# Kernel optimization log

Measured on AMD Instinct MI355X. Metric: run time of the kernel, lower is better.

## Reference

```python
import jax, jax.numpy as jnp
import numpy as np

NEG = -1.0e9  # matches the -1000000000.0 masking constant in the torch source


def setup_inputs() -> dict:
    key = jax.random.key(0)
    k1, k2, k3, k4 = jax.random.split(key, 4)
    B, N, M, D = 32, 2048, 512, 128
    sequence1 = jax.random.normal(k1, (B, N, D), dtype=jnp.float32)
    sequence2 = jax.random.normal(k2, (B, M, D), dtype=jnp.float32)
    sequence1_mask = jax.random.randint(k3, (B, N), 0, 2, dtype=jnp.int32)
    sequence2_mask = jax.random.randint(k4, (B, M), 0, 2, dtype=jnp.int32)
    return {
        "sequence1": sequence1,
        "sequence2": sequence2,
        "sequence1_mask": sequence1_mask,
        "sequence2_mask": sequence2_mask,
    }


def reference(sequence1, sequence2, sequence1_mask, sequence2_mask):
    # sequence1: [B, n, d] (context), sequence2: [B, m, d] (question)
    dt = sequence1.dtype
    m1 = sequence1_mask.astype(dt)  # [B, n]
    m2 = sequence2_mask.astype(dt)  # [B, m]

    # DotProduct similarity over the (virtually) tiled tensors -> [B, n, m].
    # Fused: no [B,n,m,d] intermediates.
    S = jnp.einsum('bnd,bmd->bnm', sequence1, sequence2)

    # masked softmax over sequence2 positions (context-to-question attention)
    a2 = jax.nn.softmax(S + (1.0 - m2)[:, None, :] * NEG, axis=-1)  # [B, n, m]
    seq1_seq2_attention = jnp.einsum('bnm,bmd->bnd', a2, sequence2)

    # one-shot question-to-context attention: masked max over m, softmax over n
    s1 = jnp.max(S * m2[:, None, :] + (1.0 - m2)[:, None, :] * NEG, axis=-1)  # [B, n]
    a1 = jax.nn.softmax(s1 + (1.0 - m1) * NEG, axis=-1)  # [B, n]
    seq2_seq1_attention = jnp.einsum('bn,bnd->bd', a1, sequence1)  # [B, d]

    return (seq1_seq2_attention, a2, seq2_seq1_attention, a1)
```

## Files before the change

kernel.cpp:

```cpp
#include <hip/hip_runtime.h>
#include <stdint.h>

#define NEGC (-1.0e9f)

typedef __attribute__((ext_vector_type(8))) short bf16x8;
typedef __attribute__((ext_vector_type(4))) float f32x4;

__device__ __align__(16) unsigned short g_S2H[32u * 512u * 128u];
__device__ __align__(16) unsigned short g_S2L[32u * 512u * 128u];
__device__ __align__(16) unsigned short g_VF[32u * 128u * 512u];
__device__ float g_a1log[32 * 2048];

__device__ __forceinline__ unsigned short f2bf(float f) {
    union { float f; unsigned int u; } v; v.f = f;
    unsigned int r = v.u + 0x7fffu + ((v.u >> 16) & 1u);
    return (unsigned short)(r >> 16);
}
__device__ __forceinline__ float bf2f(unsigned short h) {
    union { float f; unsigned int u; } v; v.u = ((unsigned int)h) << 16;
    return v.f;
}

__device__ __forceinline__ void gl_lds16(const void* g, void* l) {
    __builtin_amdgcn_global_load_lds(
        (const __attribute__((address_space(1))) unsigned int*)g,
        (__attribute__((address_space(3))) unsigned int*)l, 16, 0, 0);
}

__global__ __launch_bounds__(256) void k_prep(const float* __restrict__ seq2) {
    __shared__ unsigned short Lh[32 * 136];
    const int b = blockIdx.x >> 4, c = blockIdx.x & 15, t = threadIdx.x;
    const int m0 = c * 32;

    const float4* src = (const float4*)(seq2 + (size_t)(b * 512 + m0) * 128);
    ushort4* dh = (ushort4*)(g_S2H + (size_t)(b * 512 + m0) * 128);
    ushort4* dl = (ushort4*)(g_S2L + (size_t)(b * 512 + m0) * 128);
#pragma unroll
    for (int p = 0; p < 4; ++p) {
        int idx = p * 256 + t;
        int row = idx >> 5, c4 = idx & 31;
        float4 v = src[idx];
        float vs[4] = {v.x, v.y, v.z, v.w};
        unsigned short hh[4], ll[4];
#pragma unroll
        for (int i = 0; i < 4; ++i) { hh[i] = f2bf(vs[i]); ll[i] = f2bf(vs[i] - bf2f(hh[i])); }
        ushort4 uh{hh[0], hh[1], hh[2], hh[3]};
        ushort4 ul{ll[0], ll[1], ll[2], ll[3]};
        dh[idx] = uh;
        dl[idx] = ul;
#pragma unroll
        for (int i = 0; i < 4; ++i) Lh[row * 136 + c4 * 4 + i] = hh[i];
    }
    __syncthreads();

    {
        const int l = t & 63, q = (t >> 4) & 3, fr = t & 15;
        const int ms = m0 >> 5;
#pragma unroll
        for (int pass = 0; pass < 2; ++pass) {
            int id = pass * 4 + (t >> 6);
            int wcd = id >> 2, cc = id & 3;
            int d = wcd * 64 + cc * 16 + fr;
            unsigned short pk[8];
#pragma unroll
            for (int j = 0; j < 8; ++j) pk[j] = Lh[(q * 8 + j) * 136 + d];
            size_t chunk = (size_t)b * 65536 + (size_t)wcd * 32768
                         + (size_t)ms * 2048 + cc * 512 + l * 8;
            *(bf16x8*)(g_VF + chunk) = *(bf16x8*)pk;
        }
    }
}

#define LDS_TOTAL 32768

__global__ __launch_bounds__(256, 4) void bidir_main(
    const float* __restrict__ seq1,
    const int* __restrict__ m1, const int* __restrict__ m2,
    float* __restrict__ out0, float* __restrict__ a2out,
    float* __restrict__ out2)
{
    __shared__ __align__(16) char smem[LDS_TOTAL];

    const int t = threadIdx.x, lane = t & 63, w = t >> 6;
    const int wr = w >> 1, wc = w & 1, q = lane >> 4, fr = lane & 15;
    const int orig = blockIdx.x;
    const int swzb = (orig & 7) * 256 + (orig >> 3);
    const int b = swzb >> 6, n0 = (swzb & 63) << 5;

    float* REDm = (float*)(smem);
    float* REDs = (float*)(smem + 256);

    if (orig == 0) {
#pragma unroll
        for (int i = 0; i < 16; ++i) out2[i * 256 + t] = 0.f;
    }

    auto stageK = [&](int buf, int kt) {
        const unsigned short* sb = (w < 2) ? g_S2H : g_S2L;
        const int h = w & 1;
        const char* srcb = (const char*)(sb + (size_t)(b * 512 + h * 256 + kt * 16) * 128);
        char* dstb = smem + buf * 16384 + (w >> 1) * 8192 + h * 4096;
#pragma unroll
        for (int i = 0; i < 4; ++i) {
            int r = i * 4 + q;
            int so = r * 256 + ((fr * 16) ^ ((r & 7) << 4));
            gl_lds16(srcb + so, dstb + i * 1024);
        }
    };

    stageK(0, 0);

    bf16x8 ah[4], al[4];
    {
        const float* qp = seq1 + (size_t)(b * 2048 + n0 + wr * 16 + fr) * 128;
#pragma unroll
        for (int ks = 0; ks < 4; ++ks) {
            float4 v0 = *(const float4*)(qp + ks * 32 + q * 8);
            float4 v1 = *(const float4*)(qp + ks * 32 + q * 8 + 4);
            float vs[8] = {v0.x, v0.y, v0.z, v0.w, v1.x, v1.y, v1.z, v1.w};
            unsigned short hh[8], ll[8];
#pragma unroll
            for (int j = 0; j < 8; ++j) { hh[j] = f2bf(vs[j]); ll[j] = f2bf(vs[j] - bf2f(hh[j])); }
            ah[ks] = *(bf16x8*)hh;
            al[ks] = *(bf16x8*)ll;
        }
    }

    f32x4 acc[8][2];
#pragma unroll
    for (int i = 0; i < 8; ++i) {
        acc[i][0] = (f32x4){0.f, 0.f, 0.f, 0.f};
        acc[i][1] = (f32x4){0.f, 0.f, 0.f, 0.f};
    }

    __syncthreads();

#pragma unroll
    for (int kt = 0; kt < 16; ++kt) {
        if (kt < 15) stageK((kt + 1) & 1, kt + 1);
        {
            const char* KH = smem + (kt & 1) * 16384;
            const char* KL = KH + 8192;
            const int rrow = wc * 16 + fr;
            const int sw = (fr & 7) << 4;
            f32x4 a = acc[kt >> 1][kt & 1];
            __builtin_amdgcn_s_setprio(1);
#pragma unroll
            for (int ks = 0; ks < 4; ++ks) {
                int off = (rrow * 256 + ks * 64 + q * 16) ^ sw;
                bf16x8 bh = *(const bf16x8*)(KH + off);
                bf16x8 bl = *(const bf16x8*)(KL + off);
                a = __builtin_amdgcn_mfma_f32_16x16x32_bf16(al[ks], bh, a, 0, 0, 0);
                a = __builtin_amdgcn_mfma_f32_16x16x32_bf16(ah[ks], bl, a, 0, 0, 0);
                a = __builtin_amdgcn_mfma_f32_16x16x32_bf16(ah[ks], bh, a, 0, 0, 0);
            }
            __builtin_amdgcn_s_setprio(0);
            acc[kt >> 1][kt & 1] = a;
        }
        __syncthreads();
    }

    {
        const int* m2p = m2 + b * 512 + wc * 256 + fr;
#pragma unroll
        for (int mt = 0; mt < 8; ++mt)
#pragma unroll
            for (int s = 0; s < 2; ++s) {
                bool keep = m2p[mt * 32 + s * 16] != 0;
#pragma unroll
                for (int r = 0; r < 4; ++r)
                    acc[mt][s][r] = keep ? acc[mt][s][r] : NEGC;
            }
    }
    float rmax[4];
#pragma unroll
    for (int r = 0; r < 4; ++r) rmax[r] = NEGC;
#pragma unroll
    for (int mt = 0; mt < 8; ++mt)
#pragma unroll
        for (int s = 0; s < 2; ++s)
#pragma unroll
            for (int r = 0; r < 4; ++r) rmax[r] = fmaxf(rmax[r], acc[mt][s][r]);
#pragma unroll
    for (int off = 1; off < 16; off <<= 1)
#pragma unroll
        for (int r = 0; r < 4; ++r) rmax[r] = fmaxf(rmax[r], __shfl_xor(rmax[r], off));
    if (fr == 0) {
#pragma unroll
        for (int r = 0; r < 4; ++r) REDm[wc * 32 + wr * 16 + q * 4 + r] = rmax[r];
    }
    __syncthreads();
    float RM[4];
#pragma unroll
    for (int r = 0; r < 4; ++r) {
        int rl = wr * 16 + q * 4 + r;
        RM[r] = fmaxf(REDm[rl], REDm[32 + rl]);
    }
    if (t < 32) {
        float v = fmaxf(REDm[t], REDm[32 + t]);
        float m1v = (float)m1[b * 2048 + n0 + t];
        g_a1log[b * 2048 + n0 + t] = v + (1.0f - m1v) * NEGC;
    }
    float rs[4] = {0.f, 0.f, 0.f, 0.f};
#pragma unroll
    for (int mt = 0; mt < 8; ++mt)
#pragma unroll
        for (int s = 0; s < 2; ++s)
#pragma unroll
            for (int r = 0; r < 4; ++r) {
                float e = __expf(acc[mt][s][r] - RM[r]);
                acc[mt][s][r] = e;
                rs[r] += e;
            }
#pragma unroll
    for (int off = 1; off < 16; off <<= 1)
#pragma unroll
        for (int r = 0; r < 4; ++r) rs[r] += __shfl_xor(rs[r], off);
    if (fr == 0) {
#pragma unroll
        for (int r = 0; r < 4; ++r) REDs[wc * 32 + wr * 16 + q * 4 + r] = rs[r];
    }
    __syncthreads();
    float rinv[4];
#pragma unroll
    for (int r = 0; r < 4; ++r) {
        int rl = wr * 16 + q * 4 + r;
        rinv[r] = 1.0f / (REDs[rl] + REDs[32 + rl]);
    }
    __syncthreads();

#pragma unroll
    for (int mt = 0; mt < 8; ++mt)
#pragma unroll
        for (int s = 0; s < 2; ++s) {
            int m = wc * 256 + mt * 32 + s * 16 + fr;
#pragma unroll
            for (int r = 0; r < 4; ++r) {
                int rl = wr * 16 + q * 4 + r;
                float v = acc[mt][s][r] * rinv[r];
                a2out[(size_t)(b * 2048 + n0 + rl) * 512 + m] = v;
                int off = (rl * 1024 + m * 2) ^ ((rl & 7) << 4);
                *(unsigned short*)(smem + off) = f2bf(v);
            }
        }
    __syncthreads();

    f32x4 oacc[4];
#pragma unroll
    for (int c = 0; c < 4; ++c) oacc[c] = (f32x4){0.f, 0.f, 0.f, 0.f};

    {
        const unsigned short* vf = g_VF + (size_t)b * 65536 + (size_t)wc * 32768 + lane * 8;
        const int arow = wr * 16 + fr;
        const int asw = (fr & 7) << 4;
        __builtin_amdgcn_s_setprio(1);
#pragma unroll
        for (int ms = 0; ms < 16; ++ms) {
            bf16x8 bv[4];
#pragma unroll
            for (int c = 0; c < 4; ++c)
                bv[c] = *(const bf16x8*)(vf + ms * 2048 + c * 512);
            int aoff = (arow * 1024 + ms * 64 + q * 16) ^ asw;
            bf16x8 pa = *(const bf16x8*)(smem + aoff);
#pragma unroll
            for (int c = 0; c < 4; ++c)
                oacc[c] = __builtin_amdgcn_mfma_f32_16x16x32_bf16(pa, bv[c], oacc[c], 0, 0, 0);
        }
        __builtin_amdgcn_s_setprio(0);
    }

#pragma unroll
    for (int c = 0; c < 4; ++c)
#pragma unroll
        for (int r = 0; r < 4; ++r) {
            int rl = wr * 16 + q * 4 + r;
            int d = wc * 64 + c * 16 + fr;
            out0[(size_t)(b * 2048 + n0 + rl) * 128 + d] = oacc[c][r];
        }
}

__global__ __launch_bounds__(256) void k_gemv(const float* __restrict__ seq1,
                                              float* __restrict__ a1out,
                                              float* __restrict__ out2) {
    __shared__ float a1b[256];
    __shared__ float4 red[8][32];
    __shared__ float wred[4];
    const int bid = blockIdx.x, b = bid >> 3, ch = bid & 7, t = threadIdx.x;
    const int lane = t & 63, w = t >> 6;
    const int n0 = ch * 256;

    const float4* Lp = (const float4*)(g_a1log + (size_t)b * 2048);
    float4 La = Lp[t * 2], Lb = Lp[t * 2 + 1];
    float l[8] = {La.x, La.y, La.z, La.w, Lb.x, Lb.y, Lb.z, Lb.w};

    float lmax = l[0];
#pragma unroll
    for (int j = 1; j < 8; ++j) lmax = fmaxf(lmax, l[j]);
#pragma unroll
    for (int off = 1; off < 64; off <<= 1) lmax = fmaxf(lmax, __shfl_xor(lmax, off));
    if (lane == 0) wred[w] = lmax;
    __syncthreads();
    float bmax = fmaxf(fmaxf(wred[0], wred[1]), fmaxf(wred[2], wred[3]));

    float e[8]; float s = 0.f;
#pragma unroll
    for (int j = 0; j < 8; ++j) { e[j] = __expf(l[j] - bmax); s += e[j]; }
#pragma unroll
    for (int off = 1; off < 64; off <<= 1) s += __shfl_xor(s, off);
    __syncthreads();
    if (lane == 0) wred[w] = s;
    __syncthreads();
    float inv = 1.0f / (wred[0] + wred[1] + wred[2] + wred[3]);

    if ((t >> 5) == ch) {
        float4 w0{e[0] * inv, e[1] * inv, e[2] * inv, e[3] * inv};
        float4 w1{e[4] * inv, e[5] * inv, e[6] * inv, e[7] * inv};
        int li = (t - ch * 32) * 8;
        *(float4*)(a1b + li) = w0;
        *(float4*)(a1b + li + 4) = w1;
        float4* ao = (float4*)(a1out + (size_t)b * 2048 + t * 8);
        ao[0] = w0;
        ao[1] = w1;
    }
    __syncthreads();

    const int d4 = t & 31, sl = t >> 5;
    float4 acc{0.f, 0.f, 0.f, 0.f};
    const float4* s1 = (const float4*)(seq1 + (size_t)(b * 2048 + n0 + sl * 32) * 128);
#pragma unroll 8
    for (int j = 0; j < 32; ++j) {
        float wv = a1b[sl * 32 + j];
        float4 v = s1[j * 32 + d4];
        acc.x += wv * v.x; acc.y += wv * v.y; acc.z += wv * v.z; acc.w += wv * v.w;
    }
    red[sl][d4] = acc;
    __syncthreads();
    if (t < 32) {
        float4 s0 = red[0][t];
#pragma unroll
        for (int c = 1; c < 8; ++c) {
            float4 v = red[c][t];
            s0.x += v.x; s0.y += v.y; s0.z += v.z; s0.w += v.w;
        }
        float* dst = out2 + b * 128 + t * 4;
        atomicAdd(dst + 0, s0.x);
        atomicAdd(dst + 1, s0.y);
        atomicAdd(dst + 2, s0.z);
        atomicAdd(dst + 3, s0.w);
    }
}

extern "C" void kernel_launch(void* const* d_in, const int* in_sizes, int n_in,
                              void* d_out, int out_size, void* d_ws, size_t ws_size,
                              hipStream_t stream) {
    const float* seq1 = (const float*)d_in[0];
    const float* seq2 = (const float*)d_in[1];
    const int*   m1   = (const int*)d_in[2];
    const int*   m2   = (const int*)d_in[3];
    (void)d_ws; (void)ws_size; (void)n_in; (void)in_sizes;

    float* out  = (float*)d_out;
    float* out0 = out;
    float* a2o  = out + 8388608;
    float* o2   = out + 41943040;
    float* a1o  = out + 41947136;

    k_prep<<<dim3(512), dim3(256), 0, stream>>>(seq2);
    bidir_main<<<dim3(2048), dim3(256), 0, stream>>>(seq1, m1, m2, out0, a2o, o2);
    k_gemv<<<dim3(256), dim3(256), 0, stream>>>(seq1, a1o, o2);
}
```

Measured before the change: 79.47 us.

## Use per-wave private LDS staging for K tiles to drop block barriers

```diff
diff --git a/kernel.cpp b/kernel.cpp
--- a/kernel.cpp
+++ b/kernel.cpp
@@ -5,6 +5,10 @@
 
 typedef __attribute__((ext_vector_type(8))) short bf16x8;
 typedef __attribute__((ext_vector_type(4))) float f32x4;
+
+#define VMCNT0 asm volatile("s_waitcnt vmcnt(0)" ::: "memory")
+#define LGKMCNT0 asm volatile("s_waitcnt lgkmcnt(0)" ::: "memory")
+#define SCHED0 __builtin_amdgcn_sched_barrier(0)
 
 __device__ __align__(16) unsigned short g_S2H[32u * 512u * 128u];
 __device__ __align__(16) unsigned short g_S2L[32u * 512u * 128u];
@@ -95,20 +99,20 @@
         for (int i = 0; i < 16; ++i) out2[i * 256 + t] = 0.f;
     }
 
-    auto stageK = [&](int buf, int kt) {
-        const unsigned short* sb = (w < 2) ? g_S2H : g_S2L;
-        const int h = w & 1;
-        const char* srcb = (const char*)(sb + (size_t)(b * 512 + h * 256 + kt * 16) * 128);
-        char* dstb = smem + buf * 16384 + (w >> 1) * 8192 + h * 4096;
-#pragma unroll
-        for (int i = 0; i < 4; ++i) {
-            int r = i * 4 + q;
+    char* const mybuf = smem + w * 8192;
+    auto stagePriv = [&](int kt) {
+        const char* srcH = (const char*)(g_S2H + (size_t)(b * 512 + wc * 256 + kt * 16) * 128);
+        const char* srcL = (const char*)(g_S2L + (size_t)(b * 512 + wc * 256 + kt * 16) * 128);
+#pragma unroll
+        for (int j = 0; j < 4; ++j) {
+            int r = j * 4 + q;
             int so = r * 256 + ((fr * 16) ^ ((r & 7) << 4));
-            gl_lds16(srcb + so, dstb + i * 1024);
+            gl_lds16(srcH + so, mybuf + j * 1024);
+            gl_lds16(srcL + so, mybuf + 4096 + j * 1024);
         }
     };
 
-    stageK(0, 0);
+    stagePriv(0);
 
     bf16x8 ah[4], al[4];
     {
@@ -133,32 +137,37 @@
         acc[i][1] = (f32x4){0.f, 0.f, 0.f, 0.f};
     }
 
-    __syncthreads();
-
 #pragma unroll
     for (int kt = 0; kt < 16; ++kt) {
-        if (kt < 15) stageK((kt + 1) & 1, kt + 1);
+        VMCNT0;
+        SCHED0;
+        bf16x8 bh[4], bl[4];
         {
-            const char* KH = smem + (kt & 1) * 16384;
-            const char* KL = KH + 8192;
-            const int rrow = wc * 16 + fr;
             const int sw = (fr & 7) << 4;
+#pragma unroll
+            for (int ks = 0; ks < 4; ++ks) {
+                int off = (fr * 256 + ks * 64 + q * 16) ^ sw;
+                bh[ks] = *(const bf16x8*)(mybuf + off);
+                bl[ks] = *(const bf16x8*)(mybuf + 4096 + off);
+            }
+        }
+        LGKMCNT0;
+        SCHED0;
+        if (kt < 15) stagePriv(kt + 1);
+        {
             f32x4 a = acc[kt >> 1][kt & 1];
             __builtin_amdgcn_s_setprio(1);
 #pragma unroll
             for (int ks = 0; ks < 4; ++ks) {
-                int off = (rrow * 256 + ks * 64 + q * 16) ^ sw;
-                bf16x8 bh = *(const bf16x8*)(KH + off);
-                bf16x8 bl = *(const bf16x8*)(KL + off);
-                a = __builtin_amdgcn_mfma_f32_16x16x32_bf16(al[ks], bh, a, 0, 0, 0);
-                a = __builtin_amdgcn_mfma_f32_16x16x32_bf16(ah[ks], bl, a, 0, 0, 0);
-                a = __builtin_amdgcn_mfma_f32_16x16x32_bf16(ah[ks], bh, a, 0, 0, 0);
+                a = __builtin_amdgcn_mfma_f32_16x16x32_bf16(al[ks], bh[ks], a, 0, 0, 0);
+                a = __builtin_amdgcn_mfma_f32_16x16x32_bf16(ah[ks], bl[ks], a, 0, 0, 0);
+                a = __builtin_amdgcn_mfma_f32_16x16x32_bf16(ah[ks], bh[ks], a, 0, 0, 0);
             }
             __builtin_amdgcn_s_setprio(0);
             acc[kt >> 1][kt & 1] = a;
         }
-        __syncthreads();
-    }
+    }
+    __syncthreads();
 
     {
         const int* m2p = m2 + b * 512 + wc * 256 + fr;
```

After: 101.0 us. 27.1% more time.
